# Optimization experiments

Hardware: AMD Instinct MI355X
Metric: run time of the kernel (lower is better)

## Reference

```python
import math
import jax, jax.numpy as jnp
import numpy as np

K = 8            # kernel_size (patch length)
OUT = 8
STRIDE = 1
PAD = 0
DEPTH = 2
N = max(OUT, K)  # n_qubits = 8
PI = math.pi


def _apply_1q(state, U, wire):
    # state: [P] + [2]*N, U: [2,2] (shared) or [P,2,2] (per-patch)
    st = jnp.moveaxis(state, wire + 1, -1)
    if U.ndim == 3:
        st = jnp.einsum('pij,p...j->p...i', U, st)
    else:
        st = jnp.einsum('ij,p...j->p...i', U, st)
    return jnp.moveaxis(st, -1, wire + 1)


def _apply_cnot(state, c, t):
    # flip target-axis amplitudes on the control=1 half
    s0, s1 = jnp.split(state, 2, axis=c + 1)
    s1 = jnp.flip(s1, axis=t + 1)
    return jnp.concatenate([s0, s1], axis=c + 1)


def _rot_matrix(phi, theta, omega):
    # PennyLane Rot(phi, theta, omega) = RZ(omega) RY(theta) RZ(phi)
    c = jnp.cos(theta / 2)
    s = jnp.sin(theta / 2)
    m00 = jnp.exp(-0.5j * (phi + omega)) * c
    m01 = -jnp.exp(0.5j * (phi - omega)) * s
    m10 = jnp.exp(-0.5j * (phi - omega)) * s
    m11 = jnp.exp(0.5j * (phi + omega)) * c
    return jnp.stack([jnp.stack([m00, m01]), jnp.stack([m10, m11])]).astype(jnp.complex64)


def setup_inputs() -> dict:
    key = jax.random.key(0)
    k1, k2, k3 = jax.random.split(key, 3)
    x = jax.random.normal(k1, (8, 1, 8192), dtype=jnp.float32)
    # TorchLayer default init for angle weights: uniform in [0, 2*pi)
    weights = jax.random.uniform(k2, (DEPTH, N, 3), dtype=jnp.float32) * (2 * PI)
    bias = jax.random.normal(k3, (OUT,), dtype=jnp.float32) * 0.01
    return {"x": x, "weights": weights, "bias": bias}


def reference(x, weights, bias):
    B, C, L = x.shape
    xp = jnp.pad(x, ((0, 0), (0, 0), (PAD, PAD)))
    Lout = (L + 2 * PAD - K) // STRIDE + 1
    idx = np.arange(Lout)[:, None] * STRIDE + np.arange(K)[None, :]  # [Lout, K]
    patches = xp[:, 0, :][:, idx]                    # [B, Lout, K]
    ang = PI * jnp.tanh(patches).reshape(-1, K)      # [P, K] encoding angles
    P = ang.shape[0]

    # batched statevector |0...0>, shape [P] + [2]*N
    state = jnp.zeros((P, 2 ** N), jnp.complex64).at[:, 0].set(1.0)
    state = state.reshape((P,) + (2,) * N)

    # AngleEmbedding: RX(angle) per qubit (qubits >= K get RX(0) = identity)
    for w in range(K):
        th = ang[:, w]
        c = jnp.cos(th / 2).astype(jnp.complex64)
        s = (-1j * jnp.sin(th / 2)).astype(jnp.complex64)
        U = jnp.stack([jnp.stack([c, s], -1), jnp.stack([s, c], -1)], -2)  # [P,2,2]
        state = _apply_1q(state, U, w)

    # StronglyEntanglingLayers: Rot on each wire, then CNOT ring with range r
    for l in range(DEPTH):
        for w in range(N):
            U = _rot_matrix(weights[l, w, 0], weights[l, w, 1], weights[l, w, 2])
            state = _apply_1q(state, U, w)
        r = (l % (N - 1)) + 1
        for w in range(N):
            state = _apply_cnot(state, w, (w + r) % N)

    probs = (state.real ** 2 + state.imag ** 2).reshape(P, 2 ** N)
    d = np.arange(2 ** N)
    # <Z_i> sign of each basis state (axis 0 of the [2]*N tensor is wire 0 = MSB)
    signs = np.stack([1.0 - 2.0 * ((d >> (N - 1 - i)) & 1) for i in range(OUT)], 0).astype(np.float32)
    e = probs @ signs.T                              # [P, OUT]
    out = (e + bias).reshape(B, Lout, OUT).transpose(0, 2, 1)  # [B, OUT, Lout]
    return out
```

## Files before the change

kernel.cpp:

```cpp
#include <hip/hip_runtime.h>
#include <hip/hip_bf16.h>


#define TOTAL_PATCHES 65480
#define LOUT 8185
#define LBATCH 8192
#define NX 65536

typedef _Float16 f16x8 __attribute__((ext_vector_type(8)));
typedef float f32x4 __attribute__((ext_vector_type(4)));

static __device__ __forceinline__ unsigned short f2h_bits(float f) {
  union { _Float16 h; unsigned short u; } v;
  v.h = (_Float16)f;
  return v.u;
}

__global__ __launch_bounds__(256) void prep_all(const float* __restrict__ w,
                                                unsigned short* __restrict__ wf16) {
  __shared__ float re[256], im[256];
  const int k = blockIdx.x;
  const int t = threadIdx.x;
  re[t] = 0.f; im[t] = 0.f;
  __syncthreads();
  if (t == 0) re[k] = 1.f;
  __syncthreads();
  for (int l = 0; l < 2; ++l) {
    for (int wi = 0; wi < 8; ++wi) {
      float phi = w[(l * 8 + wi) * 3 + 0];
      float th  = w[(l * 8 + wi) * 3 + 1];
      float om  = w[(l * 8 + wi) * 3 + 2];
      float ch = cosf(0.5f * th), sh = sinf(0.5f * th);
      float aa = 0.5f * (phi + om), bb = 0.5f * (phi - om);
      float ca = cosf(aa), sa = sinf(aa), cb = cosf(bb), sb = sinf(bb);
      float m00r = ch * ca, m00i = -ch * sa;
      float m01r = -sh * cb, m01i = -sh * sb;
      float m10r = sh * cb,  m10i = -sh * sb;
      float m11r = ch * ca,  m11i = ch * sa;
      int pos = 7 - wi;
      int mask = 1 << pos;
      int lowm = mask - 1;
      if (t < 128) {
        int pp = t;
        int d0 = ((pp & ~lowm) << 1) | (pp & lowm);
        int d1 = d0 | mask;
        float a0r = re[d0], a0i = im[d0], a1r = re[d1], a1i = im[d1];
        re[d0] = m00r * a0r - m00i * a0i + m01r * a1r - m01i * a1i;
        im[d0] = m00r * a0i + m00i * a0r + m01r * a1i + m01i * a1r;
        re[d1] = m10r * a0r - m10i * a0i + m11r * a1r - m11i * a1i;
        im[d1] = m10r * a0i + m10i * a0r + m11r * a1i + m11i * a1r;
      }
      __syncthreads();
    }
    int r = (l % 7) + 1;
    for (int wi = 0; wi < 8; ++wi) {
      int c = wi, tg = (wi + r) & 7;
      int pc = 7 - c, pt = 7 - tg;
      int p1 = pc > pt ? pc : pt, p0 = pc < pt ? pc : pt;
      if (t < 64) {
        int lm0 = (1 << p0) - 1;
        int v2 = ((t & ~lm0) << 1) | (t & lm0);
        int lm1 = (1 << p1) - 1;
        int db = ((v2 & ~lm1) << 1) | (v2 & lm1);
        int d0 = db | (1 << pc);
        int d1 = d0 | (1 << pt);
        float tr = re[d0], ti = im[d0];
        re[d0] = re[d1]; im[d0] = im[d1];
        re[d1] = tr;     im[d1] = ti;
      }
      __syncthreads();
    }
  }
  int pop = __popc(k) & 3;
  for (int idx = t; idx < 512; idx += 256) {
    int n = idx;
    int d = n & 255;
    float vr = re[d], vi = im[d];
    float pr, qi;
    if (pop == 0)      { pr =  vr; qi =  vi; }
    else if (pop == 1) { pr =  vi; qi = -vr; }
    else if (pop == 2) { pr = -vr; qi = -vi; }
    else               { pr = -vi; qi =  vr; }
    float val = (n < 256) ? pr : qi;
    int off = (((k >> 5) * 32 + (n >> 4)) * 64 + ((k >> 3) & 3) * 16 + (n & 15)) * 8 + (k & 7);
    wf16[off] = f2h_bits(val);
  }
}

__global__ __launch_bounds__(1024, 1) void quanv_main(
    const float* __restrict__ x,
    const f16x8* __restrict__ wf, const float* __restrict__ bias,
    float* __restrict__ out) {
  __shared__ __align__(16) unsigned short R0[128 * 264];
  __shared__ float esm[1024];
  __shared__ float2 cssn2[144];
  const int tid = threadIdx.x;
  const int lane = tid & 63;
  const int wave = tid >> 6;
  const int pbase = blockIdx.x * 128;

  const int b0 = pbase / LOUT;
  const int base0 = b0 * LBATCH + (pbase - b0 * LOUT);
  if (tid < 144) {
    int g = base0 + tid;
    if (g > NX - 1) g = NX - 1;
    float t = tanhf(x[g]);
    float s, c;
    __sincosf(1.57079632679489662f * t, &s, &c);
    cssn2[tid] = make_float2(c, s);
  }
  __syncthreads();

  {
    int pl = tid & 31;
    int q = (tid >> 5) & 7;
    int s = tid >> 8;
    int patch = pbase + s * 32 + pl;
    if (patch > TOTAL_PATCHES - 1) patch = TOTAL_PATCHES - 1;
    int b = patch / LOUT;
    int off0 = b * LBATCH + (patch - b * LOUT) - base0;
    float fc[8], fs[8];
#pragma unroll
    for (int wq = 0; wq < 8; ++wq) {
      float2 v = cssn2[off0 + wq];
      fc[wq] = v.x; fs[wq] = v.y;
    }
    float arr[32];
    arr[0] = ((q & 4) ? fs[0] : fc[0]) * ((q & 2) ? fs[1] : fc[1]) * ((q & 1) ? fs[2] : fc[2]);
#pragma unroll
    for (int lev = 0; lev < 5; ++lev) {
      int wq = 7 - lev;
      int sz = 1 << lev;
#pragma unroll
      for (int j = 0; j < 32; ++j) {
        if (j < sz) {
          float a = arr[j];
          arr[sz + j] = a * fs[wq];
          arr[j] = a * fc[wq];
        }
      }
    }
    int mtg = s * 2 + (pl >> 4);
    int fragbase = (q * 8 + mtg) * 64 + (pl & 15);
#pragma unroll
    for (int khalf = 0; khalf < 4; ++khalf) {
      f16x8 vH;
#pragma unroll
      for (int jj = 0; jj < 8; ++jj) vH[jj] = (_Float16)arr[khalf * 8 + jj];
      *(f16x8*)&R0[(fragbase + khalf * 16) * 8] = vH;
    }
  }
  __syncthreads();

  f32x4 acc[8][2];
#pragma unroll
  for (int i = 0; i < 8; ++i)
#pragma unroll
    for (int j = 0; j < 2; ++j) acc[i][j] = (f32x4){0.f, 0.f, 0.f, 0.f};

#pragma unroll
  for (int kc = 0; kc < 8; ++kc) {
    f16x8 af[8];
#pragma unroll
    for (int mt = 0; mt < 8; ++mt)
      af[mt] = *(const f16x8*)&R0[((kc * 8 + mt) * 64 + lane) * 8];
#pragma unroll
    for (int t2 = 0; t2 < 2; ++t2) {
      int nt = (t2 == 0) ? wave : (16 + wave);
      f16x8 b = wf[(kc * 32 + nt) * 64 + lane];
#pragma unroll
      for (int mt = 0; mt < 8; ++mt)
        acc[mt][t2] = __builtin_amdgcn_mfma_f32_16x16x32_f16(af[mt], b, acc[mt][t2], 0, 0, 0);
    }
  }

  __syncthreads();
#pragma unroll
  for (int mt = 0; mt < 8; ++mt)
#pragma unroll
    for (int r = 0; r < 4; ++r) {
      float vr = acc[mt][0][r], vi = acc[mt][1][r];
      float p = vr * vr + vi * vi;
      int patch_l = mt * 16 + (lane >> 4) * 4 + r;
      int d = wave * 16 + (lane & 15);
      R0[patch_l * 264 + d] = f2h_bits(p);
    }
  __syncthreads();

  if (wave < 8) {
    f32x4 e4 = {0.f, 0.f, 0.f, 0.f};
    int io = lane & 15;
    int plr = wave * 16 + (lane & 15);
    int hi4 = lane >> 4;
#pragma unroll
    for (int kc2 = 0; kc2 < 8; ++kc2) {
      int k0 = kc2 * 32 + hi4 * 8;
      f16x8 aH = *(const f16x8*)&R0[plr * 264 + k0];
      f16x8 b2;
#pragma unroll
      for (int bb = 0; bb < 8; ++bb) {
        _Float16 sv = (_Float16)0.f;
        if (io < 8) sv = (((k0 + bb) >> (7 - io)) & 1) ? (_Float16)(-1.f) : (_Float16)(1.f);
        b2[bb] = sv;
      }
      e4 = __builtin_amdgcn_mfma_f32_16x16x32_f16(aH, b2, e4, 0, 0, 0);
    }
    if (io < 8) {
      float bv = bias[io];
#pragma unroll
      for (int r = 0; r < 4; ++r)
        esm[io * 128 + (wave * 16 + hi4 * 4 + r)] = e4[r] + bv;
    }
  }
  __syncthreads();

  {
    int io2 = tid >> 7, pl2 = tid & 127;
    int patch = pbase + pl2;
    if (patch < TOTAL_PATCHES) {
      int b = patch / LOUT;
      int l = patch - b * LOUT;
      out[(b * 8 + io2) * LOUT + l] = esm[io2 * 128 + pl2];
    }
  }
}

extern "C" void kernel_launch(void* const* d_in, const int* in_sizes, int n_in,
                              void* d_out, int out_size, void* d_ws, size_t ws_size,
                              hipStream_t stream) {
  const float* x = (const float*)d_in[0];
  const float* w = (const float*)d_in[1];
  const float* bias = (const float*)d_in[2];
  float* out = (float*)d_out;
  char* ws = (char*)d_ws;
  unsigned short* wf16 = (unsigned short*)ws;

  prep_all<<<256, 256, 0, stream>>>(w, wf16);
  quanv_main<<<512, 1024, 0, stream>>>(x, (const f16x8*)wf16, bias, out);
}
```

Baseline: 37.36 us.

## Run prep statevector simulation in registers with wave shuffles instead of LDS

The prep kernel now uses one 64-lane wave per block, with each lane holding four amplitudes in registers. Rotation gates and CNOTs exchange amplitudes through cross-lane shuffles or within-lane swaps, replacing the shared-memory updates and the __syncthreads barrier after every gate. This targets the barrier-heavy serial chain in the small prep kernel that runs before the main MFMA kernel, at the cost of more shuffle instructions and fully unrolled code.

```diff
diff --git a/kernel.cpp b/kernel.cpp
--- a/kernel.cpp
+++ b/kernel.cpp
@@ -16,16 +16,20 @@
   return v.u;
 }
 
-__global__ __launch_bounds__(256) void prep_all(const float* __restrict__ w,
-                                                unsigned short* __restrict__ wf16) {
-  __shared__ float re[256], im[256];
+__global__ __launch_bounds__(64) void prep_all(const float* __restrict__ w,
+                                               unsigned short* __restrict__ wf16) {
   const int k = blockIdx.x;
-  const int t = threadIdx.x;
-  re[t] = 0.f; im[t] = 0.f;
-  __syncthreads();
-  if (t == 0) re[k] = 1.f;
-  __syncthreads();
+  const int lane = threadIdx.x;
+  float re[4], im[4];
+#pragma unroll
+  for (int s = 0; s < 4; ++s) {
+    re[s] = (lane * 4 + s == k) ? 1.f : 0.f;
+    im[s] = 0.f;
+  }
+
+#pragma unroll
   for (int l = 0; l < 2; ++l) {
+#pragma unroll
     for (int wi = 0; wi < 8; ++wi) {
       float phi = w[(l * 8 + wi) * 3 + 0];
       float th  = w[(l * 8 + wi) * 3 + 1];
@@ -37,53 +41,67 @@
       float m01r = -sh * cb, m01i = -sh * sb;
       float m10r = sh * cb,  m10i = -sh * sb;
       float m11r = ch * ca,  m11i = ch * sa;
-      int pos = 7 - wi;
-      int mask = 1 << pos;
-      int lowm = mask - 1;
-      if (t < 128) {
-        int pp = t;
-        int d0 = ((pp & ~lowm) << 1) | (pp & lowm);
-        int d1 = d0 | mask;
-        float a0r = re[d0], a0i = im[d0], a1r = re[d1], a1i = im[d1];
-        re[d0] = m00r * a0r - m00i * a0i + m01r * a1r - m01i * a1i;
-        im[d0] = m00r * a0i + m00i * a0r + m01r * a1i + m01i * a1r;
-        re[d1] = m10r * a0r - m10i * a0i + m11r * a1r - m11i * a1i;
-        im[d1] = m10r * a0i + m10i * a0r + m11r * a1i + m11i * a1r;
-      }
-      __syncthreads();
-    }
-    int r = (l % 7) + 1;
+      const int p = 7 - wi;
+      float or_[4], oi_[4];
+#pragma unroll
+      for (int s = 0; s < 4; ++s) { or_[s] = re[s]; oi_[s] = im[s]; }
+#pragma unroll
+      for (int s = 0; s < 4; ++s) {
+        float pr_, pi_;
+        if (p >= 2) {
+          pr_ = __shfl_xor(or_[s], 1 << (p - 2), 64);
+          pi_ = __shfl_xor(oi_[s], 1 << (p - 2), 64);
+        } else {
+          pr_ = or_[s ^ (1 << p)];
+          pi_ = oi_[s ^ (1 << p)];
+        }
+        int bit = ((lane * 4 + s) >> p) & 1;
+        float cAr = bit ? m11r : m00r, cAi = bit ? m11i : m00i;
+        float cBr = bit ? m10r : m01r, cBi = bit ? m10i : m01i;
+        re[s] = cAr * or_[s] - cAi * oi_[s] + cBr * pr_ - cBi * pi_;
+        im[s] = cAr * oi_[s] + cAi * or_[s] + cBr * pi_ + cBi * pr_;
+      }
+    }
+    const int r = l + 1;
+#pragma unroll
     for (int wi = 0; wi < 8; ++wi) {
-      int c = wi, tg = (wi + r) & 7;
-      int pc = 7 - c, pt = 7 - tg;
-      int p1 = pc > pt ? pc : pt, p0 = pc < pt ? pc : pt;
-      if (t < 64) {
-        int lm0 = (1 << p0) - 1;
-        int v2 = ((t & ~lm0) << 1) | (t & lm0);
-        int lm1 = (1 << p1) - 1;
-        int db = ((v2 & ~lm1) << 1) | (v2 & lm1);
-        int d0 = db | (1 << pc);
-        int d1 = d0 | (1 << pt);
-        float tr = re[d0], ti = im[d0];
-        re[d0] = re[d1]; im[d0] = im[d1];
-        re[d1] = tr;     im[d1] = ti;
-      }
-      __syncthreads();
-    }
-  }
-  int pop = __popc(k) & 3;
-  for (int idx = t; idx < 512; idx += 256) {
-    int n = idx;
-    int d = n & 255;
-    float vr = re[d], vi = im[d];
+      const int pc = 7 - wi;
+      const int pt = 7 - ((wi + r) & 7);
+      float or_[4], oi_[4];
+#pragma unroll
+      for (int s = 0; s < 4; ++s) { or_[s] = re[s]; oi_[s] = im[s]; }
+#pragma unroll
+      for (int s = 0; s < 4; ++s) {
+        int d = lane * 4 + s;
+        int ctrl = (d >> pc) & 1;
+        if (pt >= 2) {
+          int srcl = lane ^ (ctrl << (pt - 2));
+          re[s] = __shfl(or_[s], srcl, 64);
+          im[s] = __shfl(oi_[s], srcl, 64);
+        } else {
+          float fr = or_[s ^ (1 << pt)], fi = oi_[s ^ (1 << pt)];
+          re[s] = ctrl ? fr : or_[s];
+          im[s] = ctrl ? fi : oi_[s];
+        }
+      }
+    }
+  }
+
+  const int pop = __popc(k) & 3;
+#pragma unroll
+  for (int s = 0; s < 4; ++s) {
+    int d = lane * 4 + s;
+    float vr = re[s], vi = im[s];
     float pr, qi;
     if (pop == 0)      { pr =  vr; qi =  vi; }
     else if (pop == 1) { pr =  vi; qi = -vr; }
     else if (pop == 2) { pr = -vr; qi = -vi; }
     else               { pr = -vi; qi =  vr; }
-    float val = (n < 256) ? pr : qi;
-    int off = (((k >> 5) * 32 + (n >> 4)) * 64 + ((k >> 3) & 3) * 16 + (n & 15)) * 8 + (k & 7);
-    wf16[off] = f2h_bits(val);
+    int offR = (((k >> 5) * 32 + (d >> 4)) * 64 + ((k >> 3) & 3) * 16 + (d & 15)) * 8 + (k & 7);
+    int n2 = d + 256;
+    int offI = (((k >> 5) * 32 + (n2 >> 4)) * 64 + ((k >> 3) & 3) * 16 + (n2 & 15)) * 8 + (k & 7);
+    wf16[offR] = f2h_bits(pr);
+    wf16[offI] = f2h_bits(qi);
   }
 }
 
@@ -235,6 +253,6 @@
   char* ws = (char*)d_ws;
   unsigned short* wf16 = (unsigned short*)ws;
 
-  prep_all<<<256, 256, 0, stream>>>(w, wf16);
+  prep_all<<<256, 64, 0, stream>>>(w, wf16);
   quanv_main<<<512, 1024, 0, stream>>>(x, (const f16x8*)wf16, bias, out);
 }
```

New measurement: 36.44 us, median of 2. -2.5%, faster.
